# Kernel optimization log

Measured on AMD Instinct MI355X. Metric: run time of the kernel, lower is better.

The kernel has to match this reference:

```python
import jax, jax.numpy as jnp
import numpy as np

WS = 7        # window size (square)
SH = 3        # shift size
NH = 8        # num heads
N = WS * WS   # tokens per window


def _rel_pos_index():
    coords = np.stack(np.meshgrid(np.arange(WS), np.arange(WS), indexing='ij'))
    cf = coords.reshape(2, -1)                      # (2, N)
    rel = cf[:, :, None] - cf[:, None, :]           # (2, N, N)
    rel = rel.transpose(1, 2, 0)
    rel[:, :, 0] += WS - 1
    rel[:, :, 1] += WS - 1
    rel[:, :, 0] *= 2 * WS - 1
    return rel.sum(-1)                              # (N, N) int


def _attn_mask(pH, pW):
    img = np.zeros((pH, pW), dtype=np.float32)
    h_sl = [(0, pH - WS), (pH - WS, pH - SH), (pH - SH, pH)]
    w_sl = [(0, pW - WS), (pW - WS, pW - SH), (pW - SH, pW)]
    cnt = 0
    for h0, h1 in h_sl:
        for w0, w1 in w_sl:
            img[h0:h1, w0:w1] = cnt
            cnt += 1
    m = img.reshape(pH // WS, WS, pW // WS, WS).transpose(0, 2, 1, 3).reshape(-1, N)
    diff = m[:, None, :] - m[:, :, None]            # (nw, N, N)
    return np.where(diff != 0, -100.0, 0.0).astype(np.float32)


def setup_inputs() -> dict:
    key = jax.random.key(0)
    ks = jax.random.split(key, 6)
    C = 256
    return {
        'x': jax.random.normal(ks[0], (32, 56, 56, C), dtype=jnp.float32),
        'qkv_weight': jax.random.normal(ks[1], (3 * C, C), dtype=jnp.float32) * 0.02,
        'qkv_bias': jax.random.normal(ks[2], (3 * C,), dtype=jnp.float32) * 0.02,
        'proj_weight': jax.random.normal(ks[3], (C, C), dtype=jnp.float32) * 0.02,
        'proj_bias': jax.random.normal(ks[4], (C,), dtype=jnp.float32) * 0.02,
        'rpb_table': jax.random.normal(ks[5], ((2 * WS - 1) ** 2, NH), dtype=jnp.float32) * 0.02,
    }


def reference(x, qkv_weight, qkv_bias, proj_weight, proj_bias, rpb_table):
    B, H, W, C = x.shape
    hd = C // NH
    pad_r = (WS - W % WS) % WS
    pad_b = (WS - H % WS) % WS
    xp = jnp.pad(x, ((0, 0), (0, pad_b), (0, pad_r), (0, 0)))
    pH, pW = H + pad_b, W + pad_r
    xp = jnp.roll(xp, shift=(-SH, -SH), axis=(1, 2))
    nw = (pH // WS) * (pW // WS)
    # window partition -> (B*nw, N, C)
    xw = xp.reshape(B, pH // WS, WS, pW // WS, WS, C)
    xw = xw.transpose(0, 1, 3, 2, 4, 5).reshape(B * nw, N, C)
    # qkv projection
    qkv = xw @ qkv_weight.T + qkv_bias                      # (B*nw, N, 3C)
    qkv = qkv.reshape(B * nw, N, 3, NH, hd).transpose(2, 0, 3, 1, 4)
    q, k, v = qkv[0], qkv[1], qkv[2]                        # (B*nw, NH, N, hd)
    q = q * (hd ** -0.5)
    attn = jnp.einsum('bhnd,bhmd->bhnm', q, k)              # (B*nw, NH, N, N)
    # relative position bias
    idx = jnp.asarray(_rel_pos_index())
    bias = rpb_table[idx].transpose(2, 0, 1)                # (NH, N, N)
    attn = attn + bias[None]
    # shift mask
    mask = jnp.asarray(_attn_mask(pH, pW))                  # (nw, N, N)
    attn = attn.reshape(B, nw, NH, N, N) + mask[None, :, None]
    attn = jax.nn.softmax(attn.reshape(B * nw, NH, N, N), axis=-1)
    out = jnp.einsum('bhnm,bhmd->bhnd', attn, v)            # (B*nw, NH, N, hd)
    out = out.transpose(0, 2, 1, 3).reshape(B * nw, N, C)
    out = out @ proj_weight.T + proj_bias
    # window reverse
    out = out.reshape(B, pH // WS, pW // WS, WS, WS, C)
    out = out.transpose(0, 1, 3, 2, 4, 5).reshape(B, pH, pW, C)
    out = jnp.roll(out, shift=(SH, SH), axis=(1, 2))
    return out[:, :H, :W, :]
```

## Files before the change

### kernel.cpp

```cpp
#include <hip/hip_runtime.h>
#include <hip/hip_bf16.h>

typedef __attribute__((ext_vector_type(4))) float f32x4;
typedef __attribute__((ext_vector_type(8))) short s16x8;
typedef __attribute__((ext_vector_type(4))) short s16x4;

#define LQS 520
#define FOS 260
#define VTS 72
#define LAS 264

#define OFF_A    0
#define SZ_A     (64 * LQS * 2)
#define OFF_B    (OFF_A + SZ_A)
#define SZ_B     (256 * VTS * 2)
#define OFF_ML   (OFF_B + SZ_B)
#define SZ_ML    (8 * 64 * 4)
#define SMEM_BYTES (OFF_ML + SZ_ML)

__device__ __forceinline__ unsigned cvt2bf(float a, float b) {
    unsigned r;
    asm("v_cvt_pk_bf16_f32 %0, %1, %2" : "=v"(r) : "v"(a), "v"(b));
    return r;
}

__global__ void wcvt_kernel(const float* __restrict__ qw, const float* __restrict__ pw,
                            short* __restrict__ wqkv, short* __restrict__ wproj) {
    int idx = blockIdx.x * blockDim.x + threadIdx.x;
    int stride = gridDim.x * blockDim.x;
    for (int i = idx; i < 65536; i += stride) {
        const float* src = (i < 49152) ? (qw + i * 4) : (pw + (i - 49152) * 4);
        unsigned* dst = (unsigned*)((i < 49152) ? (wqkv + i * 4) : (wproj + (i - 49152) * 4));
        const f32x4 v = *(const f32x4*)src;
        uint2 o = { cvt2bf(v.x, v.y), cvt2bf(v.z, v.w) };
        *(uint2*)dst = o;
    }
}

__global__ void bmgen_kernel(const float* __restrict__ rpb, float* __restrict__ bm) {
    int idx = blockIdx.x * blockDim.x + threadIdx.x;
    if (idx >= 131072) return;
    int j = idx & 63;
    int i = (idx >> 6) & 63;
    int h = (idx >> 12) & 7;
    int c = idx >> 15;
    int cy = c >> 1, cx = c & 1;
    float v;
    if (j >= 49) {
        v = -1e9f;
    } else {
        int ic = i > 48 ? 48 : i;
        int yi = ic / 7, xi = ic % 7;
        int yj = j / 7, xj = j % 7;
        float bias = rpb[((yi - yj + 6) * 13 + (xi - xj + 6)) * 8 + h];
        int ri = (cy ? (yi < 4 ? 1 : 2) : 0) * 3 + (cx ? (xi < 4 ? 1 : 2) : 0);
        int rj = (cy ? (yj < 4 ? 1 : 2) : 0) * 3 + (cx ? (xj < 4 ? 1 : 2) : 0);
        float mask = (ri != rj) ? -100.0f : 0.0f;
        v = (bias + mask) * 1.4426950408889634f;
    }
    bm[idx] = v;
}

__global__ __launch_bounds__(1024, 4)
void swin_kernel(const float* __restrict__ x,
                 const float* __restrict__ qkv_bias,
                 const float* __restrict__ proj_bias,
                 const short* __restrict__ wqkv,
                 const short* __restrict__ wproj,
                 const float* __restrict__ bm,
                 float* __restrict__ out) {
    __shared__ __align__(16) char smem[SMEM_BYTES];
    short* lqk   = (short*)(smem + OFF_A);
    float* lout  = (float*)(smem + OFF_A);
    short* lvt   = (short*)(smem + OFF_B);
    short* la    = (short*)(smem + OFF_B);
    float* lml   = (float*)(smem + OFF_ML);

    const int tid  = threadIdx.x;
    const int w    = tid >> 6;
    const int lane = tid & 63;
    const int il   = lane & 15;
    const int gl   = lane >> 4;
    const int hh   = w >> 1;
    const int jh   = w & 1;

    const int b   = blockIdx.x >> 6;
    const int wid = blockIdx.x & 63;
    const int wy  = wid >> 3, wx = wid & 7;

    for (int i = tid; i < 4096; i += 1024) {
        int t = i >> 6, c4 = (i & 63) << 2;
        uint2 o;
        if (t < 49) {
            int ty = t / 7, tx = t % 7;
            int R = wy * 7 + ty + 3; if (R >= 56) R -= 56;
            int C = wx * 7 + tx + 3; if (C >= 56) C -= 56;
            const f32x4 v = *(const f32x4*)(x + (((b * 56 + R) * 56 + C) << 8) + c4);
            o.x = cvt2bf(v.x, v.y); o.y = cvt2bf(v.z, v.w);
        } else {
            o.x = 0; o.y = 0;
        }
        *(uint2*)&lqk[t * LQS + c4] = o;
    }
    __syncthreads();

    {
        f32x4 acc[4][3];
        #pragma unroll
        for (int mi = 0; mi < 4; mi++)
            #pragma unroll
            for (int t = 0; t < 3; t++) acc[mi][t] = (f32x4){0.f, 0.f, 0.f, 0.f};
        for (int k0 = 0; k0 < 256; k0 += 32) {
            s16x8 a[4];
            #pragma unroll
            for (int mi = 0; mi < 4; mi++)
                a[mi] = *(const s16x8*)&lqk[(mi * 16 + il) * LQS + k0 + 8 * gl];
            #pragma unroll
            for (int t = 0; t < 3; t++) {
                s16x8 bfr = *(const s16x8*)(wqkv + (t * 256 + 16 * w + il) * 256 + k0 + 8 * gl);
                #pragma unroll
                for (int mi = 0; mi < 4; mi++)
                    acc[mi][t] = __builtin_amdgcn_mfma_f32_16x16x32_bf16(a[mi], bfr, acc[mi][t], 0, 0, 0);
            }
        }
        {
            float bv = qkv_bias[512 + 16 * w + il];
            #pragma unroll
            for (int mi = 0; mi < 4; mi++) {
                uint2 pk = { cvt2bf(acc[mi][2][0] + bv, acc[mi][2][1] + bv),
                             cvt2bf(acc[mi][2][2] + bv, acc[mi][2][3] + bv) };
                *(uint2*)&lvt[(16 * w + il) * VTS + mi * 16 + gl * 4] = pk;
            }
        }
        __syncthreads();
        {
            float bq_ = qkv_bias[16 * w + il];
            float bk_ = qkv_bias[256 + 16 * w + il];
            const float QSCL = 0.17677669529663687f * 1.4426950408889634f;
            #pragma unroll
            for (int mi = 0; mi < 4; mi++)
                #pragma unroll
                for (int r = 0; r < 4; r++) {
                    int row = mi * 16 + gl * 4 + r;
                    unsigned u = cvt2bf((acc[mi][0][r] + bq_) * QSCL, acc[mi][1][r] + bk_);
                    lqk[row * LQS + 16 * w + il] = (short)u;
                    lqk[row * LQS + 256 + 16 * w + il] = (short)(u >> 16);
                }
        }
    }
    const int cls = ((wy == 7) ? 2 : 0) + ((wx == 7) ? 1 : 0);
    const float* bmp = bm + ((cls * 8 + hh) * 64) * 64;
    f32x4 ci[2][4];
    #pragma unroll
    for (int mi = 0; mi < 2; mi++)
        #pragma unroll
        for (int ni = 0; ni < 4; ni++)
            ci[mi][ni] = *(const f32x4*)&bmp[(ni * 16 + il) * 64 + jh * 32 + mi * 16 + gl * 4];
    __syncthreads();

    f32x4 s[2][4];
    {
        s16x8 bq[4], ak[2];
        #pragma unroll
        for (int ni = 0; ni < 4; ni++)
            bq[ni] = *(const s16x8*)&lqk[(ni * 16 + il) * LQS + 32 * hh + 8 * gl];
        #pragma unroll
        for (int mi = 0; mi < 2; mi++)
            ak[mi] = *(const s16x8*)&lqk[(jh * 32 + mi * 16 + il) * LQS + 256 + 32 * hh + 8 * gl];
        #pragma unroll
        for (int mi = 0; mi < 2; mi++)
            #pragma unroll
            for (int ni = 0; ni < 4; ni++)
                s[mi][ni] = __builtin_amdgcn_mfma_f32_16x16x32_bf16(ak[mi], bq[ni], ci[mi][ni], 0, 0, 0);
    }
    float sm[4] = { 0.f, 0.f, 0.f, 0.f };
    #pragma unroll
    for (int mi = 0; mi < 2; mi++)
        #pragma unroll
        for (int ni = 0; ni < 4; ni++)
            #pragma unroll
            for (int r = 0; r < 4; r++) {
                float p = exp2f(s[mi][ni][r]);
                s[mi][ni][r] = p;
                sm[ni] += p;
            }
    #pragma unroll
    for (int ni = 0; ni < 4; ni++) {
        sm[ni] += __shfl_xor(sm[ni], 16);
        sm[ni] += __shfl_xor(sm[ni], 32);
    }
    if (jh == 0 && gl == 0) {
        #pragma unroll
        for (int ni = 0; ni < 4; ni++) lml[hh * 64 + ni * 16 + il] = sm[ni];
    }
    unsigned pkd[2][4][2];
    #pragma unroll
    for (int mi = 0; mi < 2; mi++)
        #pragma unroll
        for (int ni = 0; ni < 4; ni++) {
            pkd[mi][ni][0] = cvt2bf(s[mi][ni][0], s[mi][ni][1]);
            pkd[mi][ni][1] = cvt2bf(s[mi][ni][2], s[mi][ni][3]);
        }
    __syncthreads();

    f32x4 o[2][4];
    {
        s16x8 av[2];
        #pragma unroll
        for (int md = 0; md < 2; md++)
            av[md] = *(const s16x8*)&lvt[(32 * hh + md * 16 + il) * VTS + jh * 32 + 8 * gl];
        #pragma unroll
        for (int ni = 0; ni < 4; ni++) {
            unsigned wd[4];
            #pragma unroll
            for (int q = 0; q < 4; q++) {
                int src = (2 * (gl & 1) + (q >> 1)) * 16 + il;
                unsigned v0 = (unsigned)__shfl((int)pkd[0][ni][q & 1], src);
                unsigned v1 = (unsigned)__shfl((int)pkd[1][ni][q & 1], src);
                wd[q] = (gl & 2) ? v1 : v0;
            }
            union { unsigned u[4]; s16x8 v; } cv;
            cv.u[0] = wd[0]; cv.u[1] = wd[1]; cv.u[2] = wd[2]; cv.u[3] = wd[3];
            #pragma unroll
            for (int md = 0; md < 2; md++)
                o[md][ni] = __builtin_amdgcn_mfma_f32_16x16x32_bf16(av[md], cv.v, (f32x4){0.f,0.f,0.f,0.f}, 0, 0, 0);
        }
    }
    if (jh == 0) {
        #pragma unroll
        for (int md = 0; md < 2; md++)
            #pragma unroll
            for (int ni = 0; ni < 4; ni++)
                *(f32x4*)&lout[(ni * 16 + il) * FOS + 32 * hh + md * 16 + gl * 4] = o[md][ni];
    }
    __syncthreads();
    if (jh == 1) {
        float sc[4];
        #pragma unroll
        for (int ni = 0; ni < 4; ni++)
            sc[ni] = __builtin_amdgcn_rcpf(lml[hh * 64 + ni * 16 + il] + sm[ni]);
        #pragma unroll
        for (int md = 0; md < 2; md++)
            #pragma unroll
            for (int ni = 0; ni < 4; ni++) {
                f32x4 t = *(const f32x4*)&lout[(ni * 16 + il) * FOS + 32 * hh + md * 16 + gl * 4];
                float a0 = (t.x + o[md][ni][0]) * sc[ni];
                float a1 = (t.y + o[md][ni][1]) * sc[ni];
                float a2 = (t.z + o[md][ni][2]) * sc[ni];
                float a3 = (t.w + o[md][ni][3]) * sc[ni];
                uint2 pk = { cvt2bf(a0, a1), cvt2bf(a2, a3) };
                *(uint2*)&la[(ni * 16 + il) * LAS + 32 * hh + md * 16 + gl * 4] = pk;
            }
    }
    __syncthreads();

    {
        f32x4 acc[4];
        #pragma unroll
        for (int mi = 0; mi < 4; mi++) acc[mi] = (f32x4){0.f, 0.f, 0.f, 0.f};
        for (int k0 = 0; k0 < 256; k0 += 32) {
            s16x8 bw = *(const s16x8*)(wproj + (16 * w + il) * 256 + k0 + 8 * gl);
            #pragma unroll
            for (int mi = 0; mi < 4; mi++) {
                s16x8 a = *(const s16x8*)&la[(mi * 16 + il) * LAS + k0 + 8 * gl];
                acc[mi] = __builtin_amdgcn_mfma_f32_16x16x32_bf16(a, bw, acc[mi], 0, 0, 0);
            }
        }
        float pb = proj_bias[16 * w + il];
        float* fout = lout;
        #pragma unroll
        for (int mi = 0; mi < 4; mi++)
            #pragma unroll
            for (int r = 0; r < 4; r++) {
                int t = mi * 16 + gl * 4 + r;
                if (t < 49) fout[t * FOS + 16 * w + il] = acc[mi][r] + pb;
            }
    }
    __syncthreads();
    for (int i = tid; i < 3136; i += 1024) {
        int t = i >> 6, c4 = (i & 63) << 2;
        f32x4 v = *(const f32x4*)&lout[t * FOS + c4];
        int ty = t / 7, tx = t % 7;
        int R = wy * 7 + ty + 3; if (R >= 56) R -= 56;
        int C = wx * 7 + tx + 3; if (C >= 56) C -= 56;
        *(f32x4*)(out + (((b * 56 + R) * 56 + C) << 8) + c4) = v;
    }
}

extern "C" void kernel_launch(void* const* d_in, const int* in_sizes, int n_in,
                              void* d_out, int out_size, void* d_ws, size_t ws_size,
                              hipStream_t stream) {
    const float* x   = (const float*)d_in[0];
    const float* qw  = (const float*)d_in[1];
    const float* qb  = (const float*)d_in[2];
    const float* pw  = (const float*)d_in[3];
    const float* pb  = (const float*)d_in[4];
    const float* rpb = (const float*)d_in[5];

    short* wqkv  = (short*)d_ws;
    short* wproj = wqkv + 768 * 256;
    float* bmt   = (float*)((char*)d_ws + 524288);

    wcvt_kernel<<<128, 256, 0, stream>>>(qw, pw, wqkv, wproj);
    bmgen_kernel<<<512, 256, 0, stream>>>(rpb, bmt);
    swin_kernel<<<2048, 1024, 0, stream>>>(x, qb, pb, wqkv, wproj, bmt, (float*)d_out);
}
```

Before: 231.3 us.

## Use one wave per head, keep V in registers, shrink LDS footprint

The fused Swin window-attention kernel moves from 16 waves per block (two waves per head splitting keys) to 8 waves, one per head. Each wave now processes its keys in two halves, carrying the softmax sum and output in registers. V stays in registers and is redistributed with shuffles instead of a transposed LDS buffer. LDS shrinks to the single QK buffer, with the projection output staged in it as bf16, which drops several barriers and the cross-wave partial-sum merge. In exchange each wave needs more registers and does twice the serial work, and the final output is rounded to bf16 before being written.

```diff
diff --git a/kernel.cpp b/kernel.cpp
--- a/kernel.cpp
+++ b/kernel.cpp
@@ -4,19 +4,11 @@
 typedef __attribute__((ext_vector_type(4))) float f32x4;
 typedef __attribute__((ext_vector_type(8))) short s16x8;
 typedef __attribute__((ext_vector_type(4))) short s16x4;
+typedef __attribute__((ext_vector_type(4))) unsigned uintx4;
 
 #define LQS 520
-#define FOS 260
-#define VTS 72
-#define LAS 264
-
-#define OFF_A    0
-#define SZ_A     (64 * LQS * 2)
-#define OFF_B    (OFF_A + SZ_A)
-#define SZ_B     (256 * VTS * 2)
-#define OFF_ML   (OFF_B + SZ_B)
-#define SZ_ML    (8 * 64 * 4)
-#define SMEM_BYTES (OFF_ML + SZ_ML)
+
+#define SMEM_BYTES (64 * LQS * 2)
 
 __device__ __forceinline__ unsigned cvt2bf(float a, float b) {
     unsigned r;
@@ -61,7 +53,7 @@
     bm[idx] = v;
 }
 
-__global__ __launch_bounds__(1024, 4)
+__global__ __launch_bounds__(512, 4)
 void swin_kernel(const float* __restrict__ x,
                  const float* __restrict__ qkv_bias,
                  const float* __restrict__ proj_bias,
@@ -69,26 +61,19 @@
                  const short* __restrict__ wproj,
                  const float* __restrict__ bm,
                  float* __restrict__ out) {
-    __shared__ __align__(16) char smem[SMEM_BYTES];
-    short* lqk   = (short*)(smem + OFF_A);
-    float* lout  = (float*)(smem + OFF_A);
-    short* lvt   = (short*)(smem + OFF_B);
-    short* la    = (short*)(smem + OFF_B);
-    float* lml   = (float*)(smem + OFF_ML);
+    __shared__ __align__(16) short lqk[64 * LQS];
 
     const int tid  = threadIdx.x;
-    const int w    = tid >> 6;
+    const int h    = tid >> 6;
     const int lane = tid & 63;
     const int il   = lane & 15;
     const int gl   = lane >> 4;
-    const int hh   = w >> 1;
-    const int jh   = w & 1;
 
     const int b   = blockIdx.x >> 6;
     const int wid = blockIdx.x & 63;
     const int wy  = wid >> 3, wx = wid & 7;
 
-    for (int i = tid; i < 4096; i += 1024) {
+    for (int i = tid; i < 4096; i += 512) {
         int t = i >> 6, c4 = (i & 63) << 2;
         uint2 o;
         if (t < 49) {
@@ -104,111 +89,148 @@
     }
     __syncthreads();
 
+    unsigned pv[4][2][2];
     {
-        f32x4 acc[4][3];
+        f32x4 vacc[4][2];
         #pragma unroll
         for (int mi = 0; mi < 4; mi++)
             #pragma unroll
-            for (int t = 0; t < 3; t++) acc[mi][t] = (f32x4){0.f, 0.f, 0.f, 0.f};
+            for (int md = 0; md < 2; md++) vacc[mi][md] = (f32x4){0.f, 0.f, 0.f, 0.f};
         for (int k0 = 0; k0 < 256; k0 += 32) {
             s16x8 a[4];
             #pragma unroll
             for (int mi = 0; mi < 4; mi++)
                 a[mi] = *(const s16x8*)&lqk[(mi * 16 + il) * LQS + k0 + 8 * gl];
             #pragma unroll
-            for (int t = 0; t < 3; t++) {
-                s16x8 bfr = *(const s16x8*)(wqkv + (t * 256 + 16 * w + il) * 256 + k0 + 8 * gl);
+            for (int md = 0; md < 2; md++) {
+                s16x8 bfr = *(const s16x8*)(wqkv + (512 + 32 * h + 16 * md + il) * 256 + k0 + 8 * gl);
                 #pragma unroll
                 for (int mi = 0; mi < 4; mi++)
-                    acc[mi][t] = __builtin_amdgcn_mfma_f32_16x16x32_bf16(a[mi], bfr, acc[mi][t], 0, 0, 0);
-            }
-        }
-        {
-            float bv = qkv_bias[512 + 16 * w + il];
+                    vacc[mi][md] = __builtin_amdgcn_mfma_f32_16x16x32_bf16(a[mi], bfr, vacc[mi][md], 0, 0, 0);
+            }
+        }
+        #pragma unroll
+        for (int md = 0; md < 2; md++) {
+            float bv = qkv_bias[512 + 32 * h + 16 * md + il];
             #pragma unroll
             for (int mi = 0; mi < 4; mi++) {
-                uint2 pk = { cvt2bf(acc[mi][2][0] + bv, acc[mi][2][1] + bv),
-                             cvt2bf(acc[mi][2][2] + bv, acc[mi][2][3] + bv) };
-                *(uint2*)&lvt[(16 * w + il) * VTS + mi * 16 + gl * 4] = pk;
+                pv[mi][md][0] = cvt2bf(vacc[mi][md][0] + bv, vacc[mi][md][1] + bv);
+                pv[mi][md][1] = cvt2bf(vacc[mi][md][2] + bv, vacc[mi][md][3] + bv);
+            }
+        }
+    }
+
+    {
+        f32x4 acc[4][4];
+        #pragma unroll
+        for (int mi = 0; mi < 4; mi++)
+            #pragma unroll
+            for (int ni = 0; ni < 4; ni++) acc[mi][ni] = (f32x4){0.f, 0.f, 0.f, 0.f};
+        for (int k0 = 0; k0 < 256; k0 += 32) {
+            s16x8 a[4];
+            #pragma unroll
+            for (int mi = 0; mi < 4; mi++)
+                a[mi] = *(const s16x8*)&lqk[(mi * 16 + il) * LQS + k0 + 8 * gl];
+            #pragma unroll
+            for (int ni = 0; ni < 4; ni++) {
+                int col = (ni < 2) ? (32 * h + 16 * ni) : (256 + 32 * h + 16 * (ni - 2));
+                s16x8 bfr = *(const s16x8*)(wqkv + (col + il) * 256 + k0 + 8 * gl);
+                #pragma unroll
+                for (int mi = 0; mi < 4; mi++)
+                    acc[mi][ni] = __builtin_amdgcn_mfma_f32_16x16x32_bf16(a[mi], bfr, acc[mi][ni], 0, 0, 0);
             }
         }
         __syncthreads();
         {
-            float bq_ = qkv_bias[16 * w + il];
-            float bk_ = qkv_bias[256 + 16 * w + il];
             const float QSCL = 0.17677669529663687f * 1.4426950408889634f;
             #pragma unroll
-            for (int mi = 0; mi < 4; mi++)
+            for (int t = 0; t < 2; t++) {
+                float bq_ = qkv_bias[32 * h + 16 * t + il];
+                float bk_ = qkv_bias[256 + 32 * h + 16 * t + il];
+                #pragma unroll
+                for (int mi = 0; mi < 4; mi++)
+                    #pragma unroll
+                    for (int r = 0; r < 4; r++) {
+                        int row = mi * 16 + gl * 4 + r;
+                        unsigned u = cvt2bf((acc[mi][t][r] + bq_) * QSCL, acc[mi][t + 2][r] + bk_);
+                        lqk[row * LQS + 32 * h + 16 * t + il] = (short)u;
+                        lqk[row * LQS + 256 + 32 * h + 16 * t + il] = (short)(u >> 16);
+                    }
+            }
+        }
+    }
+
+    const int cls = ((wy == 7) ? 2 : 0) + ((wx == 7) ? 1 : 0);
+    const float* bmp = bm + ((cls * 8 + h) * 64) * 64;
+
+    s16x8 bq[4];
+    #pragma unroll
+    for (int ni = 0; ni < 4; ni++)
+        bq[ni] = *(const s16x8*)&lqk[(ni * 16 + il) * LQS + 32 * h + 8 * gl];
+
+    f32x4 o[2][4];
+    #pragma unroll
+    for (int md = 0; md < 2; md++)
+        #pragma unroll
+        for (int ni = 0; ni < 4; ni++) o[md][ni] = (f32x4){0.f, 0.f, 0.f, 0.f};
+    float l[4] = { 0.f, 0.f, 0.f, 0.f };
+
+    #pragma unroll 1
+    for (int half = 0; half < 2; half++) {
+        f32x4 s[2][4];
+        #pragma unroll
+        for (int mi = 0; mi < 2; mi++)
+            #pragma unroll
+            for (int ni = 0; ni < 4; ni++)
+                s[mi][ni] = *(const f32x4*)&bmp[(ni * 16 + il) * 64 + half * 32 + mi * 16 + gl * 4];
+        #pragma unroll
+        for (int mi = 0; mi < 2; mi++) {
+            s16x8 ak = *(const s16x8*)&lqk[(half * 32 + mi * 16 + il) * LQS + 256 + 32 * h + 8 * gl];
+            #pragma unroll
+            for (int ni = 0; ni < 4; ni++)
+                s[mi][ni] = __builtin_amdgcn_mfma_f32_16x16x32_bf16(ak, bq[ni], s[mi][ni], 0, 0, 0);
+        }
+        #pragma unroll
+        for (int mi = 0; mi < 2; mi++)
+            #pragma unroll
+            for (int ni = 0; ni < 4; ni++)
                 #pragma unroll
                 for (int r = 0; r < 4; r++) {
-                    int row = mi * 16 + gl * 4 + r;
-                    unsigned u = cvt2bf((acc[mi][0][r] + bq_) * QSCL, acc[mi][1][r] + bk_);
-                    lqk[row * LQS + 16 * w + il] = (short)u;
-                    lqk[row * LQS + 256 + 16 * w + il] = (short)(u >> 16);
+                    float p = exp2f(s[mi][ni][r]);
+                    s[mi][ni][r] = p;
+                    l[ni] += p;
                 }
-        }
-    }
-    const int cls = ((wy == 7) ? 2 : 0) + ((wx == 7) ? 1 : 0);
-    const float* bmp = bm + ((cls * 8 + hh) * 64) * 64;
-    f32x4 ci[2][4];
-    #pragma unroll
-    for (int mi = 0; mi < 2; mi++)
-        #pragma unroll
-        for (int ni = 0; ni < 4; ni++)
-            ci[mi][ni] = *(const f32x4*)&bmp[(ni * 16 + il) * 64 + jh * 32 + mi * 16 + gl * 4];
-    __syncthreads();
-
-    f32x4 s[2][4];
-    {
-        s16x8 bq[4], ak[2];
-        #pragma unroll
-        for (int ni = 0; ni < 4; ni++)
-            bq[ni] = *(const s16x8*)&lqk[(ni * 16 + il) * LQS + 32 * hh + 8 * gl];
+        unsigned pkd[2][4][2];
         #pragma unroll
         for (int mi = 0; mi < 2; mi++)
-            ak[mi] = *(const s16x8*)&lqk[(jh * 32 + mi * 16 + il) * LQS + 256 + 32 * hh + 8 * gl];
-        #pragma unroll
-        for (int mi = 0; mi < 2; mi++)
-            #pragma unroll
-            for (int ni = 0; ni < 4; ni++)
-                s[mi][ni] = __builtin_amdgcn_mfma_f32_16x16x32_bf16(ak[mi], bq[ni], ci[mi][ni], 0, 0, 0);
-    }
-    float sm[4] = { 0.f, 0.f, 0.f, 0.f };
-    #pragma unroll
-    for (int mi = 0; mi < 2; mi++)
-        #pragma unroll
-        for (int ni = 0; ni < 4; ni++)
-            #pragma unroll
-            for (int r = 0; r < 4; r++) {
-                float p = exp2f(s[mi][ni][r]);
-                s[mi][ni][r] = p;
-                sm[ni] += p;
-            }
-    #pragma unroll
-    for (int ni = 0; ni < 4; ni++) {
-        sm[ni] += __shfl_xor(sm[ni], 16);
-        sm[ni] += __shfl_xor(sm[ni], 32);
-    }
-    if (jh == 0 && gl == 0) {
-        #pragma unroll
-        for (int ni = 0; ni < 4; ni++) lml[hh * 64 + ni * 16 + il] = sm[ni];
-    }
-    unsigned pkd[2][4][2];
-    #pragma unroll
-    for (int mi = 0; mi < 2; mi++)
-        #pragma unroll
-        for (int ni = 0; ni < 4; ni++) {
-            pkd[mi][ni][0] = cvt2bf(s[mi][ni][0], s[mi][ni][1]);
-            pkd[mi][ni][1] = cvt2bf(s[mi][ni][2], s[mi][ni][3]);
-        }
-    __syncthreads();
-
-    f32x4 o[2][4];
-    {
+            #pragma unroll
+            for (int ni = 0; ni < 4; ni++) {
+                pkd[mi][ni][0] = cvt2bf(s[mi][ni][0], s[mi][ni][1]);
+                pkd[mi][ni][1] = cvt2bf(s[mi][ni][2], s[mi][ni][3]);
+            }
+        unsigned pva[2][2], pvb[2][2];
+        #pragma unroll
+        for (int md = 0; md < 2; md++)
+            #pragma unroll
+            for (int q = 0; q < 2; q++) {
+                pva[md][q] = half ? pv[2][md][q] : pv[0][md][q];
+                pvb[md][q] = half ? pv[3][md][q] : pv[1][md][q];
+            }
         s16x8 av[2];
         #pragma unroll
-        for (int md = 0; md < 2; md++)
-            av[md] = *(const s16x8*)&lvt[(32 * hh + md * 16 + il) * VTS + jh * 32 + 8 * gl];
+        for (int md = 0; md < 2; md++) {
+            unsigned wd[4];
+            #pragma unroll
+            for (int q = 0; q < 4; q++) {
+                int src = (2 * (gl & 1) + (q >> 1)) * 16 + il;
+                unsigned v0 = (unsigned)__shfl((int)pva[md][q & 1], src);
+                unsigned v1 = (unsigned)__shfl((int)pvb[md][q & 1], src);
+                wd[q] = (gl & 2) ? v1 : v0;
+            }
+            union { unsigned u[4]; s16x8 v; } cv;
+            cv.u[0] = wd[0]; cv.u[1] = wd[1]; cv.u[2] = wd[2]; cv.u[3] = wd[3];
+            av[md] = cv.v;
+        }
         #pragma unroll
         for (int ni = 0; ni < 4; ni++) {
             unsigned wd[4];
@@ -223,67 +245,80 @@
             cv.u[0] = wd[0]; cv.u[1] = wd[1]; cv.u[2] = wd[2]; cv.u[3] = wd[3];
             #pragma unroll
             for (int md = 0; md < 2; md++)
-                o[md][ni] = __builtin_amdgcn_mfma_f32_16x16x32_bf16(av[md], cv.v, (f32x4){0.f,0.f,0.f,0.f}, 0, 0, 0);
-        }
-    }
-    if (jh == 0) {
-        #pragma unroll
-        for (int md = 0; md < 2; md++)
-            #pragma unroll
-            for (int ni = 0; ni < 4; ni++)
-                *(f32x4*)&lout[(ni * 16 + il) * FOS + 32 * hh + md * 16 + gl * 4] = o[md][ni];
-    }
+                o[md][ni] = __builtin_amdgcn_mfma_f32_16x16x32_bf16(av[md], cv.v, o[md][ni], 0, 0, 0);
+        }
+    }
+    #pragma unroll
+    for (int ni = 0; ni < 4; ni++) {
+        l[ni] += __shfl_xor(l[ni], 16);
+        l[ni] += __shfl_xor(l[ni], 32);
+        l[ni] = __builtin_amdgcn_rcpf(l[ni]);
+    }
+    #pragma unroll
+    for (int md = 0; md < 2; md++)
+        #pragma unroll
+        for (int ni = 0; ni < 4; ni++) {
+            uint2 pk = { cvt2bf(o[md][ni][0] * l[ni], o[md][ni][1] * l[ni]),
+                         cvt2bf(o[md][ni][2] * l[ni], o[md][ni][3] * l[ni]) };
+            *(uint2*)&lqk[(ni * 16 + il) * LQS + 32 * h + md * 16 + gl * 4] = pk;
+        }
     __syncthreads();
-    if (jh == 1) {
-        float sc[4];
-        #pragma unroll
-        for (int ni = 0; ni < 4; ni++)
-            sc[ni] = __builtin_amdgcn_rcpf(lml[hh * 64 + ni * 16 + il] + sm[ni]);
-        #pragma unroll
-        for (int md = 0; md < 2; md++)
-            #pragma unroll
-            for (int ni = 0; ni < 4; ni++) {
-                f32x4 t = *(const f32x4*)&lout[(ni * 16 + il) * FOS + 32 * hh + md * 16 + gl * 4];
-                float a0 = (t.x + o[md][ni][0]) * sc[ni];
-                float a1 = (t.y + o[md][ni][1]) * sc[ni];
-                float a2 = (t.z + o[md][ni][2]) * sc[ni];
-                float a3 = (t.w + o[md][ni][3]) * sc[ni];
-                uint2 pk = { cvt2bf(a0, a1), cvt2bf(a2, a3) };
-                *(uint2*)&la[(ni * 16 + il) * LAS + 32 * hh + md * 16 + gl * 4] = pk;
-            }
+
+    {
+        f32x4 acc[4][2];
+        #pragma unroll
+        for (int mi = 0; mi < 4; mi++)
+            #pragma unroll
+            for (int ni = 0; ni < 2; ni++) acc[mi][ni] = (f32x4){0.f, 0.f, 0.f, 0.f};
+        for (int k0 = 0; k0 < 256; k0 += 32) {
+            s16x8 a[4];
+            #pragma unroll
+            for (int mi = 0; mi < 4; mi++)
+                a[mi] = *(const s16x8*)&lqk[(mi * 16 + il) * LQS + k0 + 8 * gl];
+            #pragma unroll
+            for (int ni = 0; ni < 2; ni++) {
+                s16x8 bw = *(const s16x8*)(wproj + (32 * h + 16 * ni + il) * 256 + k0 + 8 * gl);
+                #pragma unroll
+                for (int mi = 0; mi < 4; mi++)
+                    acc[mi][ni] = __builtin_amdgcn_mfma_f32_16x16x32_bf16(a[mi], bw, acc[mi][ni], 0, 0, 0);
+            }
+        }
+        #pragma unroll
+        for (int ni = 0; ni < 2; ni++) {
+            int oc = 32 * h + 16 * ni + il;
+            float pb = proj_bias[oc];
+            #pragma unroll
+            for (int mi = 0; mi < 4; mi++)
+                #pragma unroll
+                for (int r = 0; r < 4; r++) {
+                    int t = mi * 16 + gl * 4 + r;
+                    if (t < 49) {
+                        unsigned u = cvt2bf(acc[mi][ni][r] + pb, 0.f);
+                        lqk[t * LQS + 256 + oc] = (short)u;
+                    }
+                }
+        }
     }
     __syncthreads();
 
-    {
-        f32x4 acc[4];
-        #pragma unroll
-        for (int mi = 0; mi < 4; mi++) acc[mi] = (f32x4){0.f, 0.f, 0.f, 0.f};
-        for (int k0 = 0; k0 < 256; k0 += 32) {
-            s16x8 bw = *(const s16x8*)(wproj + (16 * w + il) * 256 + k0 + 8 * gl);
-            #pragma unroll
-            for (int mi = 0; mi < 4; mi++) {
-                s16x8 a = *(const s16x8*)&la[(mi * 16 + il) * LAS + k0 + 8 * gl];
-                acc[mi] = __builtin_amdgcn_mfma_f32_16x16x32_bf16(a, bw, acc[mi], 0, 0, 0);
-            }
-        }
-        float pb = proj_bias[16 * w + il];
-        float* fout = lout;
-        #pragma unroll
-        for (int mi = 0; mi < 4; mi++)
-            #pragma unroll
-            for (int r = 0; r < 4; r++) {
-                int t = mi * 16 + gl * 4 + r;
-                if (t < 49) fout[t * FOS + 16 * w + il] = acc[mi][r] + pb;
-            }
-    }
-    __syncthreads();
-    for (int i = tid; i < 3136; i += 1024) {
-        int t = i >> 6, c4 = (i & 63) << 2;
-        f32x4 v = *(const f32x4*)&lout[t * FOS + c4];
+    for (int i = tid; i < 1568; i += 512) {
+        int t = i >> 5, c8 = (i & 31) << 3;
+        uintx4 u = *(const uintx4*)&lqk[t * LQS + 256 + c8];
+        f32x4 v0, v1;
+        v0.x = __builtin_bit_cast(float, u.x << 16);
+        v0.y = __builtin_bit_cast(float, u.x & 0xFFFF0000u);
+        v0.z = __builtin_bit_cast(float, u.y << 16);
+        v0.w = __builtin_bit_cast(float, u.y & 0xFFFF0000u);
+        v1.x = __builtin_bit_cast(float, u.z << 16);
+        v1.y = __builtin_bit_cast(float, u.z & 0xFFFF0000u);
+        v1.z = __builtin_bit_cast(float, u.w << 16);
+        v1.w = __builtin_bit_cast(float, u.w & 0xFFFF0000u);
         int ty = t / 7, tx = t % 7;
         int R = wy * 7 + ty + 3; if (R >= 56) R -= 56;
         int C = wx * 7 + tx + 3; if (C >= 56) C -= 56;
-        *(f32x4*)(out + (((b * 56 + R) * 56 + C) << 8) + c4) = v;
+        float* op = out + (((b * 56 + R) * 56 + C) << 8) + c8;
+        *(f32x4*)op = v0;
+        *(f32x4*)(op + 4) = v1;
     }
 }
 
@@ -303,5 +338,5 @@
 
     wcvt_kernel<<<128, 256, 0, stream>>>(qw, pw, wqkv, wproj);
     bmgen_kernel<<<512, 256, 0, stream>>>(rpb, bmt);
-    swin_kernel<<<2048, 1024, 0, stream>>>(x, qb, pb, wqkv, wproj, bmt, (float*)d_out);
-}
+    swin_kernel<<<2048, 512, 0, stream>>>(x, qb, pb, wqkv, wproj, bmt, (float*)d_out);
+}
```

After: 458.5 us. 98.2% more time.
